# Kernel optimization log

Measured on AMD Instinct MI355X. Metric: run time of the kernel, lower is better.

The kernel has to match this reference:

```python
import jax, jax.numpy as jnp
import numpy as np

STRIDE = (4, 4)
MASK = (17, 17)
G_MEAN = 85.384
G_STD = 53.798
LEV = 5  # len(bins)
EPS = 1e-8
_BINS = np.array([0.0, 0.5, G_MEAN - G_STD, G_MEAN, G_MEAN + G_STD], dtype=np.float32)
_DISTS = [1, 2, 4]
_THETAS = [0.0, np.pi / 4, np.pi / 2, 3 * np.pi / 4]
# skimage greycomatrix offsets: (row, col) = (round(sin(t)*d), round(cos(t)*d)), dist-major
OFFSETS = [(int(round(np.sin(t) * d)), int(round(np.cos(t) * d))) for d in _DISTS for t in _THETAS]


def setup_inputs():
    key = jax.random.key(0)
    x = jax.random.uniform(key, (8, 1, 512, 512), dtype=jnp.float32) * 255.0
    return {"inputs": x}


def _sliding_windows(x):
    B, C, H, W = x.shape
    nx = (H - MASK[0]) // STRIDE[0] + 1
    ny = (W - MASK[1]) // STRIDE[1] + 1
    rows = (jnp.arange(nx) * STRIDE[0])[:, None] + jnp.arange(MASK[0])  # (nx, Mx)
    cols = (jnp.arange(ny) * STRIDE[1])[:, None] + jnp.arange(MASK[1])  # (ny, My)
    w = x[:, :, rows]              # (B, C, nx, Mx, W)
    w = w[:, :, :, :, cols]        # (B, C, nx, Mx, ny, My)
    return jnp.transpose(w, (0, 1, 2, 4, 3, 5))  # (B, C, nx, ny, Mx, My)


def _statistics(w):
    m = w.mean(axis=(-2, -1))
    s = w.std(axis=(-2, -1))
    mx = w.max(axis=(-2, -1))
    mn = w.min(axis=(-2, -1))
    # Faithful to original: mean is rescaled in-place BEFORE being used in max/min stats
    m = m / G_MEAN
    s = s / G_STD
    mx = (mx - m) / G_STD
    mn = (m - mn) / G_STD
    return jnp.concatenate([m, s, mx, mn], axis=1)  # (B, 4*C, nx, ny)


def _glcm(qf, dr, dc):
    # qf: (Wn, Mx, My) int32 -> normalized symmetric GLCM (Wn, LEV, LEV)
    Mx, My = qf.shape[-2:]
    if dc >= 0:
        a = qf[:, :Mx - dr, :My - dc]
        b = qf[:, dr:, dc:]
    else:
        a = qf[:, :Mx - dr, -dc:]
        b = qf[:, dr:, :My + dc]
    Wn = qf.shape[0]
    code = (a * LEV + b).reshape(Wn, -1)
    flat = (jnp.arange(Wn, dtype=jnp.int32)[:, None] * (LEV * LEV) + code).reshape(-1)
    cnt = jax.ops.segment_sum(jnp.ones(flat.shape, jnp.float32), flat, num_segments=Wn * LEV * LEV)
    G = cnt.reshape(Wn, LEV, LEV)
    G = G + jnp.swapaxes(G, -1, -2)  # symmetric=True
    return G / jnp.sum(G, axis=(-2, -1), keepdims=True)  # normed=True


def _hist_glcm_features(q):
    # q: (B, C, nx, ny, Mx, My) int32 -> (B, 64, nx, ny) (C must be 1)
    B, C, nx, ny, Mx, My = q.shape
    qf = q.reshape(-1, Mx, My)
    Wn = qf.shape[0]
    G = jnp.stack([_glcm(qf, dr, dc) for dr, dc in OFFSETS], axis=1)  # (Wn, 12, L, L)

    I = jnp.arange(LEV, dtype=jnp.float32)
    d2 = (I[:, None] - I[None, :]) ** 2
    contrast = jnp.einsum('wkij,ij->wk', G, d2)
    homogeneity = jnp.einsum('wkij,ij->wk', G, 1.0 / (1.0 + d2))
    energy = jnp.sqrt(jnp.sum(G * G, axis=(-2, -1)))
    Pi = G.sum(axis=-1)   # (Wn, 12, L)
    Pj = G.sum(axis=-2)
    mu_i = jnp.sum(I * Pi, axis=-1)
    mu_j = jnp.sum(I * Pj, axis=-1)
    di = I[None, None, :] - mu_i[..., None]
    dj = I[None, None, :] - mu_j[..., None]
    std_i = jnp.sqrt(jnp.sum(Pi * di * di, axis=-1))
    std_j = jnp.sqrt(jnp.sum(Pj * dj * dj, axis=-1))
    cov = jnp.einsum('wkij,wki,wkj->wk', G, di, dj)
    denom = std_i * std_j
    correlation = jnp.where(denom < 1e-15, 1.0, cov / jnp.maximum(denom, 1e-30))
    entropy = -jnp.sum(G * jnp.log2(G + EPS), axis=(-2, -1))  # (Wn, 12)

    qv = qf.reshape(Wn, -1)
    cnts = jnp.stack([jnp.sum(qv == k, axis=-1) for k in range(1, LEV)], axis=-1).astype(jnp.float32)
    tot = cnts.sum(axis=-1, keepdims=True)
    hist = jnp.where(tot > 0, cnts / jnp.maximum(tot, 1.0), 0.0)  # (Wn, LEV-1)

    feat = jnp.concatenate([hist, contrast, homogeneity, energy, correlation, entropy], axis=-1)
    feat = feat.reshape(B, C, nx, ny, -1)
    return jnp.transpose(feat, (0, 4, 2, 3, 1))[..., 0]  # (B, 64, nx, ny)


def reference(inputs):
    w = _sliding_windows(inputs)                                   # (B,C,nx,ny,17,17)
    stat = _statistics(w)                                          # (B,4,nx,ny)
    q = (jnp.digitize(w, jnp.asarray(_BINS)) - 1).astype(jnp.int32)
    hg = _hist_glcm_features(q)                                    # (B,64,nx,ny)
    feats = jnp.concatenate([stat, hg], axis=1)                    # (B,68,nx,ny)
    return jnp.mean(feats, axis=(-2, -1))                          # (B,68)
```

## Files before the change

kernel.cpp:

```cpp
#include <hip/hip_runtime.h>


#define G_MEAN_F 85.384f
#define G_STD_F  53.798f

__device__ constexpr int LO15[15] = {0,0,0,0,0,1,1,1,1,2,2,2,3,3,4};
__device__ constexpr int HI15[15] = {0,1,2,3,4,1,2,3,4,2,3,4,3,4,4};

__device__ __forceinline__ float wred(float v) {
#pragma unroll
  for (int m = 32; m; m >>= 1) v += __shfl_xor(v, m, 64);
  return v;
}

__device__ __forceinline__ void load_sl(const unsigned* sl, int idx, unsigned m[5]) {
  const uint4 q = *(const uint4*)(sl + idx * 4);
  m[1] = q.x; m[2] = q.y; m[3] = q.z; m[4] = q.w;
  m[0] = 0x1FFFFu & ~(m[1] | m[2] | m[3] | m[4]);
}

template<int DC>
__device__ __forceinline__ void updoff(unsigned* cnt, const unsigned a[5], const unsigned b[5]) {
  unsigned as[5], bs[5];
#pragma unroll
  for (int v = 0; v < 5; ++v) {
    as[v] = (DC < 0) ? (a[v] >> (-DC)) : a[v];
    bs[v] = (DC > 0) ? (b[v] >> DC) : b[v];
  }
#pragma unroll
  for (int u = 0; u < 15; ++u) {
    const int i = LO15[u], j = HI15[u];
    unsigned t = as[i] & bs[j];
    if (i != j) t |= as[j] & bs[i];
    cnt[u] += __popc(t);
  }
}

__device__ __forceinline__ void feat5(const unsigned* cnt, float Np,
                                      float& con, float& hom, float& ene,
                                      float& corr, float& ent) {
  const float invN = 1.0f / Np;
  const float inv2N = 0.5f / Np;
  con = 0.0f; hom = 0.0f; ent = 0.0f;
  float eac = 0.0f;
  float P[5] = {0, 0, 0, 0, 0};
#pragma unroll
  for (int u = 0; u < 15; ++u) {
    const int lo = LO15[u], hi = HI15[u];
    const float m = (float)cnt[u];
    const float d2 = (float)((hi - lo) * (hi - lo));
    con += m * d2;
    hom += m * (1.0f / (1.0f + d2));
    if (lo == hi) {
      eac += m * m;
      P[lo] += 2.0f * m;
      float g = m * invN;
      ent -= g * __log2f(g + 1e-8f);
    } else {
      eac += 0.5f * m * m;
      P[lo] += m; P[hi] += m;
      float g = m * inv2N;
      ent -= 2.0f * g * __log2f(g + 1e-8f);
    }
  }
  con *= invN;
  hom *= invN;
  ene = sqrtf(eac) * invN;
  float mu = 0.0f;
#pragma unroll
  for (int i = 0; i < 5; ++i) { P[i] *= inv2N; mu += (float)i * P[i]; }
  float s2 = 0.0f;
#pragma unroll
  for (int i = 0; i < 5; ++i) { float d = (float)i - mu; s2 = fmaf(P[i] * d, d, s2); }
  float denom = s2;
  float cov = 0.0f;
#pragma unroll
  for (int u = 0; u < 15; ++u)
    cov += ((float)cnt[u] * invN) * ((float)LO15[u] - mu) * ((float)HI15[u] - mu);
  corr = (denom < 1e-15f) ? 1.0f : cov / fmaxf(denom, 1e-30f);
}

__device__ __forceinline__ void emit2(const unsigned c1[15], const unsigned c2[15], float Np,
                                      bool v1, bool v2, float* pt0, int k0, int k1) {
  float con1, hom1, ene1, cor1, ent1, con2, hom2, ene2, cor2, ent2;
  feat5(c1, Np, con1, hom1, ene1, cor1, ent1);
  feat5(c2, Np, con2, hom2, ene2, cor2, ent2);
  if (!v1) { con1 = 0; hom1 = 0; ene1 = 0; cor1 = 0; ent1 = 0; }
  if (!v2) { con2 = 0; hom2 = 0; ene2 = 0; cor2 = 0; ent2 = 0; }
  float con = wred(con1 + con2), hom = wred(hom1 + hom2), ene = wred(ene1 + ene2);
  float cor = wred(cor1 + cor2), ent = wred(ent1 + ent2);
  if ((threadIdx.x & 63) == 0) {
    const float s = 1.0f / 15376.0f;
    pt0[(8 + k0) * 128] = con * s;
    pt0[(20 + k0) * 128] = hom * s;
    pt0[(32 + k0) * 128] = ene * s;
    pt0[(44 + k0) * 128] = cor * s;
    pt0[(56 + k0) * 128] = ent * s;
    if (k1 >= 0) {
      pt0[(8 + k1) * 128] = con * s;
      pt0[(20 + k1) * 128] = hom * s;
      pt0[(32 + k1) * 128] = ene * s;
      pt0[(44 + k1) * 128] = cor * s;
      pt0[(56 + k1) * 128] = ent * s;
    }
  }
}

template<int DR, int DC>
__device__ void glcm2(const unsigned* sl, int s, int ly, bool v1, bool v2,
                      float Np, float* pt0, int k0, int k1) {
  unsigned A[15], S[15], B[15];
#pragma unroll
  for (int u = 0; u < 15; ++u) { A[u] = 0; S[u] = 0; B[u] = 0; }
  unsigned buf[DR > 0 ? DR : 1][5];
  if constexpr (DR > 0) {
#pragma unroll
    for (int i = 0; i < DR; ++i) load_sl(sl, (s + i) * 8 + ly, buf[i]);
  }
  unsigned nxt[5];
  load_sl(sl, (s + DR) * 8 + ly, nxt);

#define SEGRUN(CNT, RB, RE)                                              \
  _Pragma("unroll 1")                                                    \
  for (int R = (RB); R < (RE); ++R) {                                    \
    unsigned cur[5];                                                     \
    _Pragma("unroll")                                                    \
    for (int v = 0; v < 5; ++v) cur[v] = nxt[v];                         \
    load_sl(sl, (s + DR + R + 1) * 8 + ly, nxt);  \
    if constexpr (DR > 0) {                                              \
      updoff<DC>(CNT, buf[0], cur);                                      \
      _Pragma("unroll")                                                  \
      for (int i = 0; i < DR - 1; ++i)                                   \
        _Pragma("unroll")                                                \
        for (int v = 0; v < 5; ++v) buf[i][v] = buf[i + 1][v];           \
      _Pragma("unroll")                                                  \
      for (int v = 0; v < 5; ++v) buf[DR > 0 ? DR - 1 : 0][v] = cur[v];  \
    } else {                                                             \
      updoff<DC>(CNT, cur, cur);                                         \
    }                                                                    \
  }

  SEGRUN(A, 0, 4)
  SEGRUN(S, 4, 17 - DR)
  SEGRUN(B, 17 - DR, 21 - DR)
#undef SEGRUN

#pragma unroll
  for (int u = 0; u < 15; ++u) { A[u] += S[u]; B[u] += S[u]; }
  emit2(A, B, Np, v1, v2, pt0, k0, k1);
}

__global__ __launch_bounds__(768)
void glcm_feat_kernel(const float* __restrict__ x,
                      float* __restrict__ part) {
  __shared__ __align__(16) unsigned sl[79 * 8 * 4];

  const int tid = threadIdx.x;
  const int lane = tid & 63;
  const int wid = tid >> 6;
  const int ty = blockIdx.x;
  const int tx = blockIdx.y;
  const int b = blockIdx.z;
  const int px0 = tx * 64;
  const int py0 = ty * 32;
  const float* xb = x + (size_t)b * 512 * 512;

  const float T1 = 0.5f;
  const float T2 = (float)(85.384 - 53.798);
  const float T3 = 85.384f;
  const float T4 = (float)(85.384 + 53.798);

  {
    const int col = py0 + lane;
    const int colc = col > 511 ? 511 : col;
#pragma unroll 1
    for (int row = wid; row < 77; row += 12) {
      int gr = px0 + row; if (gr > 511) gr = 511;
      const float xv = xb[(size_t)gr * 512 + colc];
      const int q = (int)(xv >= T1) + (int)(xv >= T2) + (int)(xv >= T3) + (int)(xv >= T4);
      const bool act = (lane < 45) && (col < 512);
      const unsigned long long b1 = __ballot(act && q == 1);
      const unsigned long long b2 = __ballot(act && q == 2);
      const unsigned long long b3 = __ballot(act && q == 3);
      const unsigned long long b4 = __ballot(act && q == 4);
      if (lane < 8) {
        const int sh4 = 4 * lane;
        const unsigned s0 = (unsigned)(b1 >> sh4) & 0x1FFFFu;
        const unsigned s1 = (unsigned)(b2 >> sh4) & 0x1FFFFu;
        const unsigned s2 = (unsigned)(b3 >> sh4) & 0x1FFFFu;
        const unsigned s3 = (unsigned)(b4 >> sh4) & 0x1FFFFu;
        *(uint4*)(sl + (row * 8 + lane) * 4) = make_uint4(s0, s1, s2, s3);
      }
    }
  }
  if (tid < 16) {
    *(uint4*)(sl + (77 * 8 + tid) * 4) = make_uint4(0u, 0u, 0u, 0u);
  }
  __syncthreads();

  const int lxp = lane >> 3, ly = lane & 7;
  const int wx1 = tx * 16 + 2 * lxp;
  const int wy = ty * 8 + ly;
  const bool vy = (wy < 124);
  const bool v1 = (wx1 < 124) && vy;
  const bool v2 = (wx1 + 1 < 124) && vy;
  const int s = 8 * lxp;
  const int tile = tx * 16 + ty;
  float* pt0 = part + (size_t)b * 68 * 128 + tile;

  if (wid == 0) {
    int sp = px0 + s; if (sp > 488) sp = 488;
    int c0 = py0 + 4 * ly; if (c0 > 492) c0 = 492;
    const float* fw = xb + (size_t)sp * 512 + c0;
    float sA = 0, qA = 0, sS = 0, qS = 0, sB = 0, qB = 0;
    float mxA = -1e30f, mnA = 1e30f, mxS = -1e30f, mnS = 1e30f, mxB = -1e30f, mnB = 1e30f;
#pragma unroll 1
    for (int r = 0; r < 21; ++r) {
      const float* p = fw + r * 512;
      const float4* p4 = (const float4*)p;
      float rs = 0, rq = 0, rmx = -1e30f, rmn = 1e30f;
#pragma unroll
      for (int w = 0; w < 4; ++w) {
        float4 f = p4[w];
        rs += f.x; rq = fmaf(f.x, f.x, rq); rmx = fmaxf(rmx, f.x); rmn = fminf(rmn, f.x);
        rs += f.y; rq = fmaf(f.y, f.y, rq); rmx = fmaxf(rmx, f.y); rmn = fminf(rmn, f.y);
        rs += f.z; rq = fmaf(f.z, f.z, rq); rmx = fmaxf(rmx, f.z); rmn = fminf(rmn, f.z);
        rs += f.w; rq = fmaf(f.w, f.w, rq); rmx = fmaxf(rmx, f.w); rmn = fminf(rmn, f.w);
      }
      float t = p[16];
      rs += t; rq = fmaf(t, t, rq); rmx = fmaxf(rmx, t); rmn = fminf(rmn, t);
      if (r < 4)       { sA += rs; qA += rq; mxA = fmaxf(mxA, rmx); mnA = fminf(mnA, rmn); }
      else if (r < 17) { sS += rs; qS += rq; mxS = fmaxf(mxS, rmx); mnS = fminf(mnS, rmn); }
      else             { sB += rs; qB += rq; mxB = fmaxf(mxB, rmx); mnB = fminf(mnB, rmn); }
    }
    float ch[4][2];
#pragma unroll
    for (int w = 0; w < 2; ++w) {
      float sum = w ? (sS + sB) : (sA + sS);
      float ssq = w ? (qS + qB) : (qA + qS);
      float mx = w ? fmaxf(mxS, mxB) : fmaxf(mxA, mxS);
      float mn = w ? fminf(mnS, mnB) : fminf(mnA, mnS);
      float mean = sum * (1.0f / 289.0f);
      float var = fmaxf(ssq * (1.0f / 289.0f) - mean * mean, 0.0f);
      float fm = mean / G_MEAN_F;
      ch[0][w] = fm;
      ch[1][w] = sqrtf(var) / G_STD_F;
      ch[2][w] = (mx - fm) / G_STD_F;
      ch[3][w] = (fm - mn) / G_STD_F;
    }
#pragma unroll
    for (int c = 0; c < 4; ++c) {
      float f = (v1 ? ch[c][0] : 0.0f) + (v2 ? ch[c][1] : 0.0f);
      f = wred(f);
      if (lane == 0) pt0[c * 128] = f * (1.0f / 15376.0f);
    }
  } else if (wid == 1) {
    unsigned hA[4] = {0,0,0,0}, hS[4] = {0,0,0,0}, hB[4] = {0,0,0,0};
#pragma unroll 1
    for (int R = 0; R < 21; ++R) {
      const uint4 q = *(const uint4*)(sl + ((s + R) * 8 + ly) * 4);
      unsigned* h = (R < 4) ? hA : (R < 17) ? hS : hB;
      h[0] += __popc(q.x); h[1] += __popc(q.y); h[2] += __popc(q.z); h[3] += __popc(q.w);
    }
    float ch[4][2];
#pragma unroll
    for (int w = 0; w < 2; ++w) {
      unsigned t1 = w ? (hS[0] + hB[0]) : (hA[0] + hS[0]);
      unsigned t2 = w ? (hS[1] + hB[1]) : (hA[1] + hS[1]);
      unsigned t3 = w ? (hS[2] + hB[2]) : (hA[2] + hS[2]);
      unsigned t4 = w ? (hS[3] + hB[3]) : (hA[3] + hS[3]);
      unsigned tot = t1 + t2 + t3 + t4;
      float ti = (tot > 0) ? 1.0f / (float)tot : 0.0f;
      ch[0][w] = (float)t1 * ti;
      ch[1][w] = (float)t2 * ti;
      ch[2][w] = (float)t3 * ti;
      ch[3][w] = (float)t4 * ti;
    }
#pragma unroll
    for (int c = 0; c < 4; ++c) {
      float f = (v1 ? ch[c][0] : 0.0f) + (v2 ? ch[c][1] : 0.0f);
      f = wred(f);
      if (lane == 0) pt0[(4 + c) * 128] = f * (1.0f / 15376.0f);
    }
  } else if (wid == 2) {
    glcm2<0, 1>(sl, s, ly, v1, v2, 272.0f, pt0, 0, -1);
  } else if (wid == 3) {
    glcm2<1, 0>(sl, s, ly, v1, v2, 272.0f, pt0, 2, -1);
  } else if (wid == 4) {
    glcm2<0, 2>(sl, s, ly, v1, v2, 255.0f, pt0, 4, -1);
  } else if (wid == 5) {
    glcm2<1, 1>(sl, s, ly, v1, v2, 256.0f, pt0, 1, 5);
  } else if (wid == 6) {
    glcm2<0, 4>(sl, s, ly, v1, v2, 221.0f, pt0, 8, -1);
  } else if (wid == 7) {
    glcm2<1, -1>(sl, s, ly, v1, v2, 256.0f, pt0, 3, 7);
  } else if (wid == 8) {
    glcm2<2, 0>(sl, s, ly, v1, v2, 255.0f, pt0, 6, -1);
  } else if (wid == 9) {
    glcm2<3, 3>(sl, s, ly, v1, v2, 196.0f, pt0, 9, -1);
  } else if (wid == 10) {
    glcm2<4, 0>(sl, s, ly, v1, v2, 221.0f, pt0, 10, -1);
  } else {
    glcm2<3, -3>(sl, s, ly, v1, v2, 196.0f, pt0, 11, -1);
  }
}

__global__ __launch_bounds__(64)
void reduce_kernel(const float* __restrict__ part, float* __restrict__ out) {
  const int ch = blockIdx.x;
  const int b = blockIdx.y;
  const int lane = threadIdx.x;
  const float2* p = (const float2*)(part + ((size_t)b * 68 + ch) * 128);
  float2 f = p[lane];
  float v = f.x + f.y;
  v = wred(v);
  if (lane == 0) out[b * 68 + ch] = v;
}

extern "C" void kernel_launch(void* const* d_in, const int* in_sizes, int n_in,
                              void* d_out, int out_size, void* d_ws, size_t ws_size,
                              hipStream_t stream)
{
  const float* x = (const float*)d_in[0];
  float* out = (float*)d_out;
  float* part = (float*)d_ws;

  glcm_feat_kernel<<<dim3(16, 8, 8), dim3(768), 0, stream>>>(x, part);
  reduce_kernel<<<dim3(68, 8), dim3(64), 0, stream>>>(part, out);
}
```

Measured before the change: 111.1 us.

## Fuse final reduction into main kernel via last-block atomic counter; batch loads

```diff
diff --git a/kernel.cpp b/kernel.cpp
--- a/kernel.cpp
+++ b/kernel.cpp
@@ -3,6 +3,7 @@
 
 #define G_MEAN_F 85.384f
 #define G_STD_F  53.798f
+#define PART_BYTES (8u * 68u * 128u * 4u)
 
 __device__ constexpr int LO15[15] = {0,0,0,0,0,1,1,1,1,2,2,2,3,3,4};
 __device__ constexpr int HI15[15] = {0,1,2,3,4,1,2,3,4,2,3,4,3,4,4};
@@ -152,8 +153,11 @@
 
 __global__ __launch_bounds__(768)
 void glcm_feat_kernel(const float* __restrict__ x,
-                      float* __restrict__ part) {
+                      float* __restrict__ part,
+                      unsigned* __restrict__ cnt,
+                      float* __restrict__ out) {
   __shared__ __align__(16) unsigned sl[79 * 8 * 4];
+  __shared__ unsigned last_flag;
 
   const int tid = threadIdx.x;
   const int lane = tid & 63;
@@ -173,23 +177,32 @@
   {
     const int col = py0 + lane;
     const int colc = col > 511 ? 511 : col;
-#pragma unroll 1
-    for (int row = wid; row < 77; row += 12) {
+    const bool act = (lane < 45) && (col < 512);
+    float xv[7];
+#pragma unroll
+    for (int i = 0; i < 7; ++i) {
+      int row = wid + 12 * i; if (row > 76) row = 76;
       int gr = px0 + row; if (gr > 511) gr = 511;
-      const float xv = xb[(size_t)gr * 512 + colc];
-      const int q = (int)(xv >= T1) + (int)(xv >= T2) + (int)(xv >= T3) + (int)(xv >= T4);
-      const bool act = (lane < 45) && (col < 512);
-      const unsigned long long b1 = __ballot(act && q == 1);
-      const unsigned long long b2 = __ballot(act && q == 2);
-      const unsigned long long b3 = __ballot(act && q == 3);
-      const unsigned long long b4 = __ballot(act && q == 4);
-      if (lane < 8) {
-        const int sh4 = 4 * lane;
-        const unsigned s0 = (unsigned)(b1 >> sh4) & 0x1FFFFu;
-        const unsigned s1 = (unsigned)(b2 >> sh4) & 0x1FFFFu;
-        const unsigned s2 = (unsigned)(b3 >> sh4) & 0x1FFFFu;
-        const unsigned s3 = (unsigned)(b4 >> sh4) & 0x1FFFFu;
-        *(uint4*)(sl + (row * 8 + lane) * 4) = make_uint4(s0, s1, s2, s3);
+      xv[i] = xb[(size_t)gr * 512 + colc];
+    }
+#pragma unroll
+    for (int i = 0; i < 7; ++i) {
+      const int row = wid + 12 * i;
+      if (row < 77) {
+        const float v = xv[i];
+        const int q = (int)(v >= T1) + (int)(v >= T2) + (int)(v >= T3) + (int)(v >= T4);
+        const unsigned long long b1 = __ballot(act && q == 1);
+        const unsigned long long b2 = __ballot(act && q == 2);
+        const unsigned long long b3 = __ballot(act && q == 3);
+        const unsigned long long b4 = __ballot(act && q == 4);
+        if (lane < 8) {
+          const int sh4 = 4 * lane;
+          const unsigned s0 = (unsigned)(b1 >> sh4) & 0x1FFFFu;
+          const unsigned s1 = (unsigned)(b2 >> sh4) & 0x1FFFFu;
+          const unsigned s2 = (unsigned)(b3 >> sh4) & 0x1FFFFu;
+          const unsigned s3 = (unsigned)(b4 >> sh4) & 0x1FFFFu;
+          *(uint4*)(sl + (row * 8 + lane) * 4) = make_uint4(s0, s1, s2, s3);
+        }
       }
     }
   }
@@ -303,18 +316,24 @@
   } else {
     glcm2<3, -3>(sl, s, ly, v1, v2, 196.0f, pt0, 11, -1);
   }
-}
-
-__global__ __launch_bounds__(64)
-void reduce_kernel(const float* __restrict__ part, float* __restrict__ out) {
-  const int ch = blockIdx.x;
-  const int b = blockIdx.y;
-  const int lane = threadIdx.x;
-  const float2* p = (const float2*)(part + ((size_t)b * 68 + ch) * 128);
-  float2 f = p[lane];
-  float v = f.x + f.y;
-  v = wred(v);
-  if (lane == 0) out[b * 68 + ch] = v;
+
+  __syncthreads();
+  if (tid == 0) {
+    unsigned old = __hip_atomic_fetch_add(&cnt[b], 1u, __ATOMIC_ACQ_REL,
+                                          __HIP_MEMORY_SCOPE_AGENT);
+    last_flag = (old == 127u) ? 1u : 0u;
+  }
+  __syncthreads();
+  if (last_flag) {
+#pragma unroll 1
+    for (int ch = wid; ch < 68; ch += 12) {
+      const float2* p = (const float2*)(part + ((size_t)b * 68 + ch) * 128);
+      float2 f = p[lane];
+      float v = f.x + f.y;
+      v = wred(v);
+      if (lane == 0) out[b * 68 + ch] = v;
+    }
+  }
 }
 
 extern "C" void kernel_launch(void* const* d_in, const int* in_sizes, int n_in,
@@ -324,7 +343,8 @@
   const float* x = (const float*)d_in[0];
   float* out = (float*)d_out;
   float* part = (float*)d_ws;
-
-  glcm_feat_kernel<<<dim3(16, 8, 8), dim3(768), 0, stream>>>(x, part);
-  reduce_kernel<<<dim3(68, 8), dim3(64), 0, stream>>>(part, out);
-}
+  unsigned* cnt = (unsigned*)((char*)d_ws + PART_BYTES);
+
+  hipMemsetAsync(cnt, 0, 8 * sizeof(unsigned), stream);
+  glcm_feat_kernel<<<dim3(16, 8, 8), dim3(768), 0, stream>>>(x, part, cnt, out);
+}
```

New measurement: 130.7 us. +17.7%, slower.
